# Performance work log

Hardware: AMD Instinct MI355X
Metric: run time of the kernel (lower is better)

Reference implementation:

```python
import jax, jax.numpy as jnp
import numpy as np

HEADS = 16


def _linear(x, w, b):
    # torch nn.Linear: y = x @ W^T + b, W: (out, in)
    return jnp.einsum('bld,od->blo', x, w) + b


def setup_inputs() -> dict:
    key = jax.random.key(0)
    ks = jax.random.split(key, 11)
    B, L, QD, KVD = 8, 2048, 1024, 1024
    s_in = 1.0 / np.sqrt(QD)
    return {
        'query': jax.random.normal(ks[0], (B, L, QD), jnp.float32),
        'key':   jax.random.normal(ks[1], (B, L, KVD), jnp.float32),
        'value': jax.random.normal(ks[2], (B, L, KVD), jnp.float32),
        'wq_w': jax.random.normal(ks[3], (KVD, QD), jnp.float32) * s_in,
        'wq_b': jnp.zeros((KVD,), jnp.float32),
        'wk_w': jax.random.normal(ks[4], (KVD, KVD), jnp.float32) * s_in,
        'wk_b': jnp.zeros((KVD,), jnp.float32),
        'wv_w': jax.random.normal(ks[5], (KVD, KVD), jnp.float32) * s_in,
        'wv_b': jnp.zeros((KVD,), jnp.float32),
        'fo_w': jax.random.normal(ks[6], (QD, KVD), jnp.float32) * s_in,
        'fo_b': jnp.zeros((QD,), jnp.float32),
    }


def reference(query, key, value, wq_w, wq_b, wk_w, wk_b, wv_w, wv_b, fo_w, fo_b):
    B, Lq, _ = query.shape
    Lk = key.shape[1]
    kvd = wq_w.shape[0]
    head_dim = kvd // HEADS
    # reshape WITHOUT transpose, exactly as the torch source: (B, L, heads, head_dim)
    q = _linear(query, wq_w, wq_b).reshape(B, Lq, HEADS, head_dim)
    k = _linear(key,   wk_w, wk_b).reshape(B, Lk, HEADS, head_dim)
    v = _linear(value, wv_w, wv_b).reshape(B, Lk, HEADS, head_dim)
    scale = 1.0 / jnp.sqrt(jnp.float32(head_dim))
    # Faithful to source: seq axis acts as 'h'; heads axis is contracted (i,j).
    scores = jnp.einsum('bhid,bhjd->bhij', q, k) * scale  # (B, L, heads, heads)
    weights = jax.nn.softmax(scores, axis=-1)
    out = jnp.einsum('bhij,bhjd->bhid', weights, v)       # (B, L, heads, head_dim)
    out = out.reshape(B, Lq, kvd)
    return _linear(out, fo_w, fo_b)
```

## Files before the change

kernel.cpp:

```cpp
#include <hip/hip_runtime.h>
#include <hip/hip_bf16.h>


typedef __attribute__((ext_vector_type(8))) __bf16 bf16x8;
typedef __attribute__((ext_vector_type(4))) float f32x4;

#define BM 128
#define BN 128
#define BK 64

__device__ __forceinline__ float bf2f(ushort u) {
  union { unsigned int i; float f; } c; c.i = ((unsigned int)u) << 16; return c.f;
}
__device__ __forceinline__ ushort f2b(float f) {
  union { float f; unsigned int i; } c; c.f = f;
  unsigned int x = c.i;
  return (ushort)((x + 0x7FFFu + ((x >> 16) & 1u)) >> 16);
}

__global__ __launch_bounds__(256)
void cvt_f32_bf16(const float* __restrict__ s, ushort* __restrict__ d, int n8)
{
  int i = blockIdx.x * 256 + threadIdx.x;
  if (i >= n8) return;
  const float4* sp = reinterpret_cast<const float4*>(s) + (size_t)i * 2;
  float4 a = sp[0], b = sp[1];
  ushort u[8] = { f2b(a.x), f2b(a.y), f2b(a.z), f2b(a.w),
                  f2b(b.x), f2b(b.y), f2b(b.z), f2b(b.w) };
  reinterpret_cast<uint4*>(d)[i] = *reinterpret_cast<uint4*>(u);
}

template<bool OUT_BF16>
__global__ __launch_bounds__(512, 2)
void gemm8p(const ushort* __restrict__ A, const ushort* __restrict__ Bw,
            const float* __restrict__ bias, void* __restrict__ Cv,
            int M, int N, int K)
{
  extern __shared__ ushort lds[];

  const int tid  = threadIdx.x;
  const int lane = tid & 63;
  const int wid  = tid >> 6;
  const int wm   = wid >> 2;
  const int wn   = wid & 3;

  const int nwg = gridDim.x * gridDim.y;
  int fid = blockIdx.y * gridDim.x + blockIdx.x;
  if ((nwg & 7) == 0) fid = (fid & 7) * (nwg >> 3) + (fid >> 3);
  const int bx = fid % gridDim.x;
  const int by = fid / gridDim.x;
  const int m0 = by * 256, n0 = bx * 256;

  const int NT = K >> 6;

  const int csw = ((lane & 7) ^ (lane >> 3)) << 3;
  auto STAGE = [&](int h, int kt, int b) {
    const ushort* base = (h >= 2) ? Bw : A;
    const int o0 = (h >= 2) ? n0 : m0;
    const int rl = (h & 1) * 128;
    #pragma unroll
    for (int j = 0; j < 2; ++j) {
      int rt = rl + j * 64 + wid * 8;
      const ushort* src = base + (size_t)(o0 + rt + (lane >> 3)) * K + kt * 64 + csw;
      ushort* dst = lds + b * 32768 + (h >= 2 ? 16384 : 0) + rt * 64;
      __builtin_amdgcn_global_load_lds(
          (const __attribute__((address_space(1))) void*)src,
          (__attribute__((address_space(3))) void*)dst, 16, 0, 0);
    }
  };

  auto LDA = [&](int b, int mi, int kk) -> bf16x8 {
    int row  = (mi & 3) * 16 + wm * 64 + (mi >> 2) * 128 + (lane & 15);
    int slot = kk * 4 + (lane >> 4);
    int byte = row * 128 + (((slot ^ (row & 7)) & 7) << 4);
    return *reinterpret_cast<const bf16x8*>((const char*)(lds + b * 32768) + byte);
  };
  auto LDB = [&](int b, int ni, int kk) -> bf16x8 {
    int row  = (ni & 1) * 16 + wn * 32 + (ni >> 1) * 128 + (lane & 15);
    int slot = kk * 4 + (lane >> 4);
    int byte = row * 128 + (((slot ^ (row & 7)) & 7) << 4);
    return *reinterpret_cast<const bf16x8*>((const char*)(lds + b * 32768 + 16384) + byte);
  };

  f32x4 acc[8][4] = {};
  bf16x8 af[4][2], bf[4][2];

  STAGE(0, 0, 0); STAGE(2, 0, 0); STAGE(3, 0, 0); STAGE(1, 0, 0);
  asm volatile("s_waitcnt vmcnt(4)" ::: "memory");
  __builtin_amdgcn_s_barrier();

  for (int t = 0; t < NT; ++t) {
    const int cur = t & 1;
    const int nxt = cur ^ 1;
    const bool pf = (t + 1) < NT;

    #pragma unroll
    for (int i = 0; i < 4; ++i) { af[i][0] = LDA(cur, i, 0); af[i][1] = LDA(cur, i, 1); }
    #pragma unroll
    for (int n = 0; n < 2; ++n) { bf[n][0] = LDB(cur, n, 0); bf[n][1] = LDB(cur, n, 1); }
    if (pf) { STAGE(0, t + 1, nxt); asm volatile("s_waitcnt vmcnt(4)" ::: "memory"); }
    else    {                       asm volatile("s_waitcnt vmcnt(2)" ::: "memory"); }
    __builtin_amdgcn_s_barrier();
    asm volatile("s_waitcnt lgkmcnt(0)" ::: "memory");
    __builtin_amdgcn_sched_barrier(0);
    __builtin_amdgcn_s_setprio(1);
    #pragma unroll
    for (int i = 0; i < 4; ++i)
      #pragma unroll
      for (int n = 0; n < 2; ++n)
        #pragma unroll
        for (int kk = 0; kk < 2; ++kk)
          acc[i][n] = __builtin_amdgcn_mfma_f32_16x16x32_bf16(af[i][kk], bf[n][kk], acc[i][n], 0, 0, 0);
    __builtin_amdgcn_s_setprio(0);
    __builtin_amdgcn_s_barrier();

    #pragma unroll
    for (int n = 0; n < 2; ++n) { bf[2 + n][0] = LDB(cur, 2 + n, 0); bf[2 + n][1] = LDB(cur, 2 + n, 1); }
    if (pf) { STAGE(2, t + 1, nxt); asm volatile("s_waitcnt vmcnt(4)" ::: "memory"); }
    else    {                       asm volatile("s_waitcnt vmcnt(0)" ::: "memory"); }
    __builtin_amdgcn_s_barrier();
    asm volatile("s_waitcnt lgkmcnt(0)" ::: "memory");
    __builtin_amdgcn_sched_barrier(0);
    __builtin_amdgcn_s_setprio(1);
    #pragma unroll
    for (int i = 0; i < 4; ++i)
      #pragma unroll
      for (int n = 0; n < 2; ++n)
        #pragma unroll
        for (int kk = 0; kk < 2; ++kk)
          acc[i][2 + n] = __builtin_amdgcn_mfma_f32_16x16x32_bf16(af[i][kk], bf[2 + n][kk], acc[i][2 + n], 0, 0, 0);
    __builtin_amdgcn_s_setprio(0);
    __builtin_amdgcn_s_barrier();

    #pragma unroll
    for (int i = 0; i < 4; ++i) { af[i][0] = LDA(cur, 4 + i, 0); af[i][1] = LDA(cur, 4 + i, 1); }
    if (pf) STAGE(3, t + 1, nxt);
    __builtin_amdgcn_s_barrier();
    asm volatile("s_waitcnt lgkmcnt(0)" ::: "memory");
    __builtin_amdgcn_sched_barrier(0);
    __builtin_amdgcn_s_setprio(1);
    #pragma unroll
    for (int i = 0; i < 4; ++i)
      #pragma unroll
      for (int n = 0; n < 2; ++n)
        #pragma unroll
        for (int kk = 0; kk < 2; ++kk)
          acc[4 + i][n] = __builtin_amdgcn_mfma_f32_16x16x32_bf16(af[i][kk], bf[n][kk], acc[4 + i][n], 0, 0, 0);
    __builtin_amdgcn_s_setprio(0);
    __builtin_amdgcn_s_barrier();

    if (pf) { STAGE(1, t + 1, nxt); asm volatile("s_waitcnt vmcnt(4)" ::: "memory"); }
    __builtin_amdgcn_s_barrier();
    __builtin_amdgcn_s_setprio(1);
    #pragma unroll
    for (int i = 0; i < 4; ++i)
      #pragma unroll
      for (int n = 0; n < 2; ++n)
        #pragma unroll
        for (int kk = 0; kk < 2; ++kk)
          acc[4 + i][2 + n] = __builtin_amdgcn_mfma_f32_16x16x32_bf16(af[i][kk], bf[2 + n][kk], acc[4 + i][2 + n], 0, 0, 0);
    __builtin_amdgcn_s_setprio(0);
    __builtin_amdgcn_s_barrier();
  }

  #pragma unroll
  for (int ni = 0; ni < 4; ++ni) {
    int col = n0 + (ni & 1) * 16 + wn * 32 + (ni >> 1) * 128 + (lane & 15);
    float bv = bias[col];
    #pragma unroll
    for (int mi = 0; mi < 8; ++mi) {
      int row0 = m0 + (mi & 3) * 16 + wm * 64 + (mi >> 2) * 128 + ((lane >> 4) << 2);
      #pragma unroll
      for (int q = 0; q < 4; ++q) {
        float v = acc[mi][ni][q] + bv;
        if constexpr (OUT_BF16)
          ((ushort*)Cv)[(size_t)(row0 + q) * N + col] = f2b(v);
        else
          ((float*)Cv)[(size_t)(row0 + q) * N + col] = v;
      }
    }
  }
}

template<bool A_IS_BF16, bool OUT_BF16>
__global__ __launch_bounds__(256)
void gemm_bt(const void* __restrict__ Av, const float* __restrict__ B,
             const float* __restrict__ bias, void* __restrict__ Cv,
             int M, int N, int K)
{
  __shared__ ushort As[BM * BK];
  __shared__ ushort Bs[BN * BK];

  const int tid  = threadIdx.x;
  const int lane = tid & 63;
  const int wid  = tid >> 6;
  const int wr   = wid >> 1;
  const int wc   = wid & 1;
  const int m0   = blockIdx.y * BM;
  const int n0   = blockIdx.x * BN;

  f32x4 acc[4][4] = {};

  const int r   = tid >> 1;
  const int seg = (tid & 1) * 32;

  for (int k0 = 0; k0 < K; k0 += BK) {
    {
      ushort tmp[32];
      if constexpr (A_IS_BF16) {
        const ushort* gA = (const ushort*)Av + (size_t)(m0 + r) * K + k0 + seg;
        #pragma unroll
        for (int u = 0; u < 4; ++u)
          *reinterpret_cast<uint4*>(&tmp[u * 8]) =
              *reinterpret_cast<const uint4*>(gA + u * 8);
      } else {
        const float* gA = (const float*)Av + (size_t)(m0 + r) * K + k0 + seg;
        #pragma unroll
        for (int u = 0; u < 8; ++u) {
          float4 f = *reinterpret_cast<const float4*>(gA + u * 4);
          tmp[u * 4 + 0] = f2b(f.x); tmp[u * 4 + 1] = f2b(f.y);
          tmp[u * 4 + 2] = f2b(f.z); tmp[u * 4 + 3] = f2b(f.w);
        }
      }
      #pragma unroll
      for (int s4 = 0; s4 < 4; ++s4) {
        int slot = (seg >> 3) + s4;
        int byte = r * 128 + ((slot ^ (r & 7)) << 4);
        *reinterpret_cast<uint4*>((char*)As + byte) =
            *reinterpret_cast<uint4*>(&tmp[s4 * 8]);
      }
    }
    {
      const float* gB = B + (size_t)(n0 + r) * K + k0 + seg;
      ushort tmp[32];
      #pragma unroll
      for (int u = 0; u < 8; ++u) {
        float4 f = *reinterpret_cast<const float4*>(gB + u * 4);
        tmp[u * 4 + 0] = f2b(f.x); tmp[u * 4 + 1] = f2b(f.y);
        tmp[u * 4 + 2] = f2b(f.z); tmp[u * 4 + 3] = f2b(f.w);
      }
      #pragma unroll
      for (int s4 = 0; s4 < 4; ++s4) {
        int slot = (seg >> 3) + s4;
        int byte = r * 128 + ((slot ^ (r & 7)) << 4);
        *reinterpret_cast<uint4*>((char*)Bs + byte) =
            *reinterpret_cast<uint4*>(&tmp[s4 * 8]);
      }
    }
    __syncthreads();

    #pragma unroll
    for (int kk = 0; kk < 2; ++kk) {
      const int kbase = kk * 32 + ((lane >> 4) << 3);
      const int slot  = kbase >> 3;
      bf16x8 af[4], bfr[4];
      #pragma unroll
      for (int mi = 0; mi < 4; ++mi) {
        int row = wr * 64 + mi * 16 + (lane & 15);
        af[mi] = *reinterpret_cast<const bf16x8*>(
            (const char*)As + row * 128 + ((slot ^ (row & 7)) << 4));
      }
      #pragma unroll
      for (int ni = 0; ni < 4; ++ni) {
        int row = wc * 64 + ni * 16 + (lane & 15);
        bfr[ni] = *reinterpret_cast<const bf16x8*>(
            (const char*)Bs + row * 128 + ((slot ^ (row & 7)) << 4));
      }
      #pragma unroll
      for (int mi = 0; mi < 4; ++mi)
        #pragma unroll
        for (int ni = 0; ni < 4; ++ni)
          acc[mi][ni] = __builtin_amdgcn_mfma_f32_16x16x32_bf16(
              af[mi], bfr[ni], acc[mi][ni], 0, 0, 0);
    }
    __syncthreads();
  }

  #pragma unroll
  for (int ni = 0; ni < 4; ++ni) {
    int col = n0 + wc * 64 + ni * 16 + (lane & 15);
    float bv = bias[col];
    #pragma unroll
    for (int mi = 0; mi < 4; ++mi) {
      int row0 = m0 + wr * 64 + mi * 16 + ((lane >> 4) << 2);
      #pragma unroll
      for (int q = 0; q < 4; ++q) {
        float v = acc[mi][ni][q] + bv;
        if constexpr (OUT_BF16)
          ((ushort*)Cv)[(size_t)(row0 + q) * N + col] = f2b(v);
        else
          ((float*)Cv)[(size_t)(row0 + q) * N + col] = v;
      }
    }
  }
}

__global__ __launch_bounds__(256)
void attn_kernel(const ushort* __restrict__ Q, const ushort* __restrict__ Kh,
                 const ushort* __restrict__ V, ushort* __restrict__ O)
{
  __shared__ float smem[4][3][16][68];
  const int tid  = threadIdx.x;
  const int wid  = tid >> 6;
  const int lane = tid & 63;
  const size_t p = (size_t)blockIdx.x * 4 + wid;

  {
    const ushort* srcs[3] = { Q + p * 1024, Kh + p * 1024, V + p * 1024 };
    const int i  = lane >> 2;
    const int d0 = (lane & 3) * 16;
    #pragma unroll
    for (int m = 0; m < 3; ++m) {
      const ushort* s = srcs[m] + lane * 16;
      ushort u[16];
      *reinterpret_cast<uint4*>(&u[0]) = *reinterpret_cast<const uint4*>(s);
      *reinterpret_cast<uint4*>(&u[8]) = *reinterpret_cast<const uint4*>(s + 8);
      #pragma unroll
      for (int e = 0; e < 16; ++e) smem[wid][m][i][d0 + e] = bf2f(u[e]);
    }
  }
  __syncthreads();

  const int i  = lane >> 2;
  const int jg = lane & 3;
  const float* qrow = smem[wid][0][i];
  const float* k0r = smem[wid][1][jg * 4 + 0];
  const float* k1r = smem[wid][1][jg * 4 + 1];
  const float* k2r = smem[wid][1][jg * 4 + 2];
  const float* k3r = smem[wid][1][jg * 4 + 3];

  float s0 = 0.f, s1 = 0.f, s2 = 0.f, s3 = 0.f;
  #pragma unroll
  for (int d = 0; d < 64; ++d) {
    float qv = qrow[d];
    s0 += qv * k0r[d]; s1 += qv * k1r[d];
    s2 += qv * k2r[d]; s3 += qv * k3r[d];
  }
  const float scale = 0.125f;
  s0 *= scale; s1 *= scale; s2 *= scale; s3 *= scale;

  float mx = fmaxf(fmaxf(s0, s1), fmaxf(s2, s3));
  mx = fmaxf(mx, __shfl_xor(mx, 1));
  mx = fmaxf(mx, __shfl_xor(mx, 2));
  float e0 = __expf(s0 - mx), e1 = __expf(s1 - mx);
  float e2 = __expf(s2 - mx), e3 = __expf(s3 - mx);
  float sum = e0 + e1 + e2 + e3;
  sum += __shfl_xor(sum, 1);
  sum += __shfl_xor(sum, 2);
  float inv = 1.0f / sum;
  e0 *= inv; e1 *= inv; e2 *= inv; e3 *= inv;

  const float* v0r = smem[wid][2][jg * 4 + 0];
  const float* v1r = smem[wid][2][jg * 4 + 1];
  const float* v2r = smem[wid][2][jg * 4 + 2];
  const float* v3r = smem[wid][2][jg * 4 + 3];
  ushort* orow = O + p * 1024 + i * 64;

  #pragma unroll
  for (int c = 0; c < 4; ++c) {
    float po[16];
    #pragma unroll
    for (int dd = 0; dd < 16; ++dd) {
      int d = c * 16 + dd;
      po[dd] = e0 * v0r[d] + e1 * v1r[d] + e2 * v2r[d] + e3 * v3r[d];
    }
    #pragma unroll
    for (int dd = 0; dd < 16; ++dd) {
      po[dd] += __shfl_xor(po[dd], 1);
      po[dd] += __shfl_xor(po[dd], 2);
    }
    if (jg == c) {
      #pragma unroll
      for (int dd = 0; dd < 16; ++dd) orow[c * 16 + dd] = f2b(po[dd]);
    }
  }
}

extern "C" void kernel_launch(void* const* d_in, const int* in_sizes, int n_in,
                              void* d_out, int out_size, void* d_ws, size_t ws_size,
                              hipStream_t stream)
{
  const float* query = (const float*)d_in[0];
  const float* key_  = (const float*)d_in[1];
  const float* value = (const float*)d_in[2];
  const float* wq_w  = (const float*)d_in[3];
  const float* wq_b  = (const float*)d_in[4];
  const float* wk_w  = (const float*)d_in[5];
  const float* wk_b  = (const float*)d_in[6];
  const float* wv_w  = (const float*)d_in[7];
  const float* wv_b  = (const float*)d_in[8];
  const float* fo_w  = (const float*)d_in[9];
  const float* fo_b  = (const float*)d_in[10];

  const int K = 1024, N = 1024;
  const int M = in_sizes[0] / K;
  const size_t slot = (size_t)M * N;
  const size_t wsl  = (size_t)N * K;
  const size_t need = (4 * slot + 4 * wsl) * sizeof(ushort);

  if (ws_size >= need && (M % 256) == 0) {
    hipFuncSetAttribute(reinterpret_cast<const void*>(gemm8p<true>),
                        hipFuncAttributeMaxDynamicSharedMemorySize, 131072);
    hipFuncSetAttribute(reinterpret_cast<const void*>(gemm8p<false>),
                        hipFuncAttributeMaxDynamicSharedMemorySize, 131072);

    ushort* S0 = (ushort*)d_ws;
    ushort* S1 = S0 + slot;
    ushort* S2 = S1 + slot;
    ushort* S3 = S2 + slot;
    ushort* Wq = S3 + slot;
    ushort* Wk = Wq + wsl;
    ushort* Wv = Wk + wsl;
    ushort* Wo = Wv + wsl;

    const int n8w = (int)(wsl / 8);
    const int n8s = (int)(slot / 8);
    dim3 g8(N / 256, M / 256);
    dim3 b8(512);

    cvt_f32_bf16<<<dim3((n8w + 255) / 256), dim3(256), 0, stream>>>(wq_w, Wq, n8w);
    cvt_f32_bf16<<<dim3((n8w + 255) / 256), dim3(256), 0, stream>>>(wk_w, Wk, n8w);
    cvt_f32_bf16<<<dim3((n8w + 255) / 256), dim3(256), 0, stream>>>(wv_w, Wv, n8w);
    cvt_f32_bf16<<<dim3((n8w + 255) / 256), dim3(256), 0, stream>>>(fo_w, Wo, n8w);

    cvt_f32_bf16<<<dim3((n8s + 255) / 256), dim3(256), 0, stream>>>(query, S0, n8s);
    gemm8p<true><<<g8, b8, 131072, stream>>>(S0, Wq, wq_b, S1, M, N, K);
    cvt_f32_bf16<<<dim3((n8s + 255) / 256), dim3(256), 0, stream>>>(key_, S0, n8s);
    gemm8p<true><<<g8, b8, 131072, stream>>>(S0, Wk, wk_b, S2, M, N, K);
    cvt_f32_bf16<<<dim3((n8s + 255) / 256), dim3(256), 0, stream>>>(value, S0, n8s);
    gemm8p<true><<<g8, b8, 131072, stream>>>(S0, Wv, wv_b, S3, M, N, K);

    attn_kernel<<<dim3(M / 4), dim3(256), 0, stream>>>(S1, S2, S3, S0);
    gemm8p<false><<<g8, b8, 131072, stream>>>(S0, Wo, fo_b, d_out, M, N, K);
  } else {
    dim3 grid(N / BN, M / BM);
    ushort* Qb = (ushort*)d_ws;
    ushort* Kb = Qb + slot;
    ushort* Vb = Kb + slot;
    ushort* Ob = Vb + slot;
    gemm_bt<false, true><<<grid, dim3(256), 0, stream>>>(query, wq_w, wq_b, Qb, M, N, K);
    gemm_bt<false, true><<<grid, dim3(256), 0, stream>>>(key_,  wk_w, wk_b, Kb, M, N, K);
    gemm_bt<false, true><<<grid, dim3(256), 0, stream>>>(value, wv_w, wv_b, Vb, M, N, K);
    attn_kernel<<<dim3(M / 4), dim3(256), 0, stream>>>(Qb, Kb, Vb, Ob);
    gemm_bt<true, false><<<grid, dim3(256), 0, stream>>>(Ob, fo_w, fo_b, d_out, M, N, K);
  }
}
```

Measured before the change: 272.0 us.

## Compute tiny per-position attention with MFMA using transposed V and permuted output weights

Replaces the scalar/LDS attention kernel with a wave-per-position MFMA kernel: QK^T and weights·V are each done with 16x16x32 bf16 MFMAs. To feed the second MFMA, the V projection GEMM writes its output in a transposed (d-major) layout. The attention output is then stored in a permuted layout, which is compensated by permuting the output-projection weight columns during its bf16 conversion. This removes the LDS staging and shuffle-heavy scalar work, at the cost of coupled layout changes across three kernels and strided scattered stores in the V GEMM epilogue.

```diff
diff --git a/kernel.cpp b/kernel.cpp
--- a/kernel.cpp
+++ b/kernel.cpp
@@ -30,7 +30,23 @@
   reinterpret_cast<uint4*>(d)[i] = *reinterpret_cast<uint4*>(u);
 }
 
-template<bool OUT_BF16>
+__global__ __launch_bounds__(256)
+void cvt_wo_perm(const float* __restrict__ w, ushort* __restrict__ o)
+{
+  int t = blockIdx.x * 256 + threadIdx.x;
+  int n  = t >> 7;
+  int i8 = (t & 127) << 3;
+  int blk = i8 >> 8, g = (i8 >> 6) & 3, i = (i8 >> 2) & 15;
+  const float* src = w + (size_t)n * 1024;
+  int c = blk * 16 + g * 4;
+  float4 a = *reinterpret_cast<const float4*>(src + i * 64 + c);
+  float4 b = *reinterpret_cast<const float4*>(src + (i + 1) * 64 + c);
+  ushort u[8] = { f2b(a.x), f2b(a.y), f2b(a.z), f2b(a.w),
+                  f2b(b.x), f2b(b.y), f2b(b.z), f2b(b.w) };
+  *reinterpret_cast<uint4*>(o + (size_t)n * 1024 + i8) = *reinterpret_cast<uint4*>(u);
+}
+
+template<int CMODE>
 __global__ __launch_bounds__(512, 2)
 void gemm8p(const ushort* __restrict__ A, const ushort* __restrict__ Bw,
             const float* __restrict__ bias, void* __restrict__ Cv,
@@ -173,11 +189,75 @@
       #pragma unroll
       for (int q = 0; q < 4; ++q) {
         float v = acc[mi][ni][q] + bv;
-        if constexpr (OUT_BF16)
+        if constexpr (CMODE == 0)
+          ((float*)Cv)[(size_t)(row0 + q) * N + col] = v;
+        else if constexpr (CMODE == 1)
           ((ushort*)Cv)[(size_t)(row0 + q) * N + col] = f2b(v);
         else
-          ((float*)Cv)[(size_t)(row0 + q) * N + col] = v;
-      }
+          ((ushort*)Cv)[(size_t)(row0 + q) * N + ((col & 63) << 4) + (col >> 6)] = f2b(v);
+      }
+    }
+  }
+}
+
+__global__ __launch_bounds__(256)
+void attn_mfma(const ushort* __restrict__ Q, const ushort* __restrict__ Kh,
+               const ushort* __restrict__ Vt, ushort* __restrict__ Ot, int P)
+{
+  const int lane = threadIdx.x & 63;
+  const int wid  = threadIdx.x >> 6;
+  const int g = lane >> 4, c = lane & 15;
+  const int stride = gridDim.x * 4;
+
+  for (int p = blockIdx.x * 4 + wid; p < P; p += stride) {
+    const ushort* qb = Q  + (size_t)p * 1024;
+    const ushort* kb = Kh + (size_t)p * 1024;
+    const ushort* vb = Vt + (size_t)p * 1024;
+
+    bf16x8 qf0 = *reinterpret_cast<const bf16x8*>(qb + c * 64 + g * 8);
+    bf16x8 qf1 = *reinterpret_cast<const bf16x8*>(qb + c * 64 + 32 + g * 8);
+    bf16x8 kf0 = *reinterpret_cast<const bf16x8*>(kb + c * 64 + g * 8);
+    bf16x8 kf1 = *reinterpret_cast<const bf16x8*>(kb + c * 64 + 32 + g * 8);
+
+    f32x4 s = {};
+    s = __builtin_amdgcn_mfma_f32_16x16x32_bf16(kf0, qf0, s, 0, 0, 0);
+    s = __builtin_amdgcn_mfma_f32_16x16x32_bf16(kf1, qf1, s, 0, 0, 0);
+
+    float s0 = s[0] * 0.125f, s1 = s[1] * 0.125f;
+    float s2 = s[2] * 0.125f, s3 = s[3] * 0.125f;
+    float m = fmaxf(fmaxf(s0, s1), fmaxf(s2, s3));
+    m = fmaxf(m, __shfl_xor(m, 16));
+    m = fmaxf(m, __shfl_xor(m, 32));
+    float e0 = __expf(s0 - m), e1 = __expf(s1 - m);
+    float e2 = __expf(s2 - m), e3 = __expf(s3 - m);
+    float sum = e0 + e1 + e2 + e3;
+    sum += __shfl_xor(sum, 16);
+    sum += __shfl_xor(sum, 32);
+    float r = 1.0f / sum;
+
+    uint pk0 = (uint)f2b(e0 * r) | ((uint)f2b(e1 * r) << 16);
+    uint pk1 = (uint)f2b(e2 * r) | ((uint)f2b(e3 * r) << 16);
+    int src = ((g & 1) << 5) | c;
+    uint y0 = (uint)__shfl((int)pk0, src);
+    uint y1 = (uint)__shfl((int)pk1, src);
+    uint y2 = (uint)__shfl((int)pk0, src | 16);
+    uint y3 = (uint)__shfl((int)pk1, src | 16);
+    if (g >= 2) { y0 = 0; y1 = 0; y2 = 0; y3 = 0; }
+    union { uint u[4]; bf16x8 v; } yu;
+    yu.u[0] = y0; yu.u[1] = y1; yu.u[2] = y2; yu.u[3] = y3;
+
+    ushort* ob = Ot + (size_t)p * 1024;
+    #pragma unroll
+    for (int blk = 0; blk < 4; ++blk) {
+      bf16x8 vf = {};
+      if (g < 2)
+        vf = *reinterpret_cast<const bf16x8*>(vb + blk * 256 + c * 16 + g * 8);
+      f32x4 o = {};
+      o = __builtin_amdgcn_mfma_f32_16x16x32_bf16(vf, yu.v, o, 0, 0, 0);
+      uint lo = (uint)f2b(o[0]) | ((uint)f2b(o[1]) << 16);
+      uint hi = (uint)f2b(o[2]) | ((uint)f2b(o[3]) << 16);
+      uint2 w2; w2.x = lo; w2.y = hi;
+      *reinterpret_cast<uint2*>(ob + blk * 256 + g * 64 + c * 4) = w2;
     }
   }
 }
@@ -357,11 +437,11 @@
   ushort* orow = O + p * 1024 + i * 64;
 
   #pragma unroll
-  for (int c = 0; c < 4; ++c) {
+  for (int cc = 0; cc < 4; ++cc) {
     float po[16];
     #pragma unroll
     for (int dd = 0; dd < 16; ++dd) {
-      int d = c * 16 + dd;
+      int d = cc * 16 + dd;
       po[dd] = e0 * v0r[d] + e1 * v1r[d] + e2 * v2r[d] + e3 * v3r[d];
     }
     #pragma unroll
@@ -369,9 +449,9 @@
       po[dd] += __shfl_xor(po[dd], 1);
       po[dd] += __shfl_xor(po[dd], 2);
     }
-    if (jg == c) {
-      #pragma unroll
-      for (int dd = 0; dd < 16; ++dd) orow[c * 16 + dd] = f2b(po[dd]);
+    if (jg == cc) {
+      #pragma unroll
+      for (int dd = 0; dd < 16; ++dd) orow[cc * 16 + dd] = f2b(po[dd]);
     }
   }
 }
@@ -398,10 +478,12 @@
   const size_t wsl  = (size_t)N * K;
   const size_t need = (4 * slot + 4 * wsl) * sizeof(ushort);
 
-  if (ws_size >= need && (M % 256) == 0) {
-    hipFuncSetAttribute(reinterpret_cast<const void*>(gemm8p<true>),
+  if (ws_size >= need && (M % 256) == 0 && N == 1024 && K == 1024) {
+    hipFuncSetAttribute(reinterpret_cast<const void*>(gemm8p<0>),
                         hipFuncAttributeMaxDynamicSharedMemorySize, 131072);
-    hipFuncSetAttribute(reinterpret_cast<const void*>(gemm8p<false>),
+    hipFuncSetAttribute(reinterpret_cast<const void*>(gemm8p<1>),
+                        hipFuncAttributeMaxDynamicSharedMemorySize, 131072);
+    hipFuncSetAttribute(reinterpret_cast<const void*>(gemm8p<2>),
                         hipFuncAttributeMaxDynamicSharedMemorySize, 131072);
 
     ushort* S0 = (ushort*)d_ws;
@@ -421,17 +503,17 @@
     cvt_f32_bf16<<<dim3((n8w + 255) / 256), dim3(256), 0, stream>>>(wq_w, Wq, n8w);
     cvt_f32_bf16<<<dim3((n8w + 255) / 256), dim3(256), 0, stream>>>(wk_w, Wk, n8w);
     cvt_f32_bf16<<<dim3((n8w + 255) / 256), dim3(256), 0, stream>>>(wv_w, Wv, n8w);
-    cvt_f32_bf16<<<dim3((n8w + 255) / 256), dim3(256), 0, stream>>>(fo_w, Wo, n8w);
+    cvt_wo_perm <<<dim3(512), dim3(256), 0, stream>>>(fo_w, Wo);
 
     cvt_f32_bf16<<<dim3((n8s + 255) / 256), dim3(256), 0, stream>>>(query, S0, n8s);
-    gemm8p<true><<<g8, b8, 131072, stream>>>(S0, Wq, wq_b, S1, M, N, K);
+    gemm8p<1><<<g8, b8, 131072, stream>>>(S0, Wq, wq_b, S1, M, N, K);
     cvt_f32_bf16<<<dim3((n8s + 255) / 256), dim3(256), 0, stream>>>(key_, S0, n8s);
-    gemm8p<true><<<g8, b8, 131072, stream>>>(S0, Wk, wk_b, S2, M, N, K);
+    gemm8p<1><<<g8, b8, 131072, stream>>>(S0, Wk, wk_b, S2, M, N, K);
     cvt_f32_bf16<<<dim3((n8s + 255) / 256), dim3(256), 0, stream>>>(value, S0, n8s);
-    gemm8p<true><<<g8, b8, 131072, stream>>>(S0, Wv, wv_b, S3, M, N, K);
-
-    attn_kernel<<<dim3(M / 4), dim3(256), 0, stream>>>(S1, S2, S3, S0);
-    gemm8p<false><<<g8, b8, 131072, stream>>>(S0, Wo, fo_b, d_out, M, N, K);
+    gemm8p<2><<<g8, b8, 131072, stream>>>(S0, Wv, wv_b, S3, M, N, K);
+
+    attn_mfma<<<dim3(2048), dim3(256), 0, stream>>>(S1, S2, S3, S0, M);
+    gemm8p<0><<<g8, b8, 131072, stream>>>(S0, Wo, fo_b, d_out, M, N, K);
   } else {
     dim3 grid(N / BN, M / BM);
     ushort* Qb = (ushort*)d_ws;
```

After: 279.6 us. +2.8%, slower.
